# Optimization experiments

Measured on AMD Instinct MI355X. Metric: run time of the kernel, lower is better.

## Reference

```python
import jax, jax.numpy as jnp
import numpy as np

N_E = 8192
DIM = 256
BETA = 0.25


def _l2norm(x, eps=1e-12):
    # matches F.normalize(p=2, dim=-1): x / max(||x||, eps)
    n = jnp.sqrt(jnp.sum(x * x, axis=-1, keepdims=True))
    return x / jnp.maximum(n, eps)


def setup_inputs() -> dict:
    key = jax.random.key(0)
    k1, k2 = jax.random.split(key)
    z = jax.random.normal(k1, (8, 1024, DIM), dtype=jnp.float32)
    embedding_weight = jax.random.normal(k2, (N_E, DIM), dtype=jnp.float32)
    return {"z": z, "embedding_weight": embedding_weight}


def reference(z, embedding_weight):
    z = _l2norm(z)                                   # [B,S,D]
    zf = z.reshape(-1, DIM)                          # [N,D]
    embed_norm = _l2norm(embedding_weight)           # [n_e,D]
    # d = ||z||^2 + ||e||^2 - 2 z.e  -> [N, n_e]
    d = (jnp.sum(zf * zf, axis=1, keepdims=True)
         + jnp.sum(embed_norm * embed_norm, axis=1)
         - 2.0 * jnp.einsum('bd,nd->bn', zf, embed_norm))
    encoding_indices = jnp.argmin(d, axis=1).reshape(z.shape[:-1])  # [B,S]
    z_q = embedding_weight[encoding_indices]          # gather raw codes
    z_q = _l2norm(z_q)                                # [B,S,D]
    loss = (BETA * jnp.mean((jax.lax.stop_gradient(z_q) - z) ** 2)
            + jnp.mean((z_q - jax.lax.stop_gradient(z)) ** 2))
    z_q = z + jax.lax.stop_gradient(z_q - z)          # straight-through
    return z_q, loss, encoding_indices
```

## Files before the change

### kernel.cpp

```cpp
#include <hip/hip_runtime.h>
#include <hip/hip_fp16.h>
#include <cfloat>
#include <math.h>

#define DIM    256
#define N_TOK  8192
#define N_E    8192
#define NSEG   1024
#define MARGIN 0.012f

typedef __attribute__((ext_vector_type(8))) short bf16x8;
typedef __attribute__((ext_vector_type(4))) float f32x4;
typedef __attribute__((ext_vector_type(8))) unsigned short ushort8;

__device__ __forceinline__ unsigned short f2bf(float f) {
    unsigned u = __float_as_uint(f);
    unsigned r = u + 0x7fff + ((u >> 16) & 1);
    return (unsigned short)(r >> 16);
}
__device__ __forceinline__ unsigned fkey(float f) {
    unsigned u = __float_as_uint(f);
    return (u & 0x80000000u) ? ~u : (u | 0x80000000u);
}
__device__ __forceinline__ unsigned short f2h(float f) {
    const __half h = __float2half(f);
    return *(const unsigned short*)&h;
}
__device__ __forceinline__ float h2f(unsigned short u) {
    __half_raw r; r.x = u;
    return __half2float((__half)r);
}

__global__ __launch_bounds__(256) void l2norm_all(const float* __restrict__ z,
                                                  const float* __restrict__ emb,
                                                  float* __restrict__ zn,
                                                  unsigned short* __restrict__ zsw,
                                                  float* __restrict__ en,
                                                  unsigned short* __restrict__ esw,
                                                  float* __restrict__ e2) {
    const int lane = threadIdx.x & 63;
    const bool isE = blockIdx.x < (N_E / 4);
    const int row = (isE ? blockIdx.x : blockIdx.x - N_E / 4) * 4 + (threadIdx.x >> 6);
    const float* in = isE ? emb : z;
    float* out = isE ? en : zn;
    unsigned short* outb = isE ? esw : zsw;
    const float4 v = *(const float4*)(in + row * DIM + lane * 4);
    float s = v.x * v.x + v.y * v.y + v.z * v.z + v.w * v.w;
#pragma unroll
    for (int off = 1; off < 64; off <<= 1) s += __shfl_xor(s, off, 64);
    const float inv = 1.0f / fmaxf(sqrtf(s), 1e-12f);
    const float4 o = make_float4(v.x * inv, v.y * inv, v.z * inv, v.w * inv);
    *(float4*)(out + row * DIM + lane * 4) = o;
    ushort4 ob; ob.x = f2bf(o.x); ob.y = f2bf(o.y); ob.z = f2bf(o.z); ob.w = f2bf(o.w);
    {
        const int k0 = lane * 4;
        const size_t sidx = ((size_t)((row >> 4) * 8 + (k0 >> 5)) * 64
                             + ((k0 >> 3) & 3) * 16 + (row & 15)) * 8 + (k0 & 7);
        *(ushort4*)(outb + sidx) = ob;
    }
    if (isE) {
        float q = o.x * o.x + o.y * o.y + o.z * o.z + o.w * o.w;
#pragma unroll
        for (int off = 1; off < 64; off <<= 1) q += __shfl_xor(q, off, 64);
        if (lane == 0) e2[row] = q;
    }
}

__global__ __launch_bounds__(256, 3) void mfma_dist(const unsigned short* __restrict__ zsw,
                                                    const unsigned short* __restrict__ esw,
                                                    const float* __restrict__ e2,
                                                    unsigned short* __restrict__ segMh) {
    __shared__ float sm[16][128];

    const int tid  = threadIdx.x;
    const int lane = tid & 63;
    const int wave = tid >> 6;
    const int wm = wave & 1, wn = wave >> 1;
    const int row0 = (blockIdx.x & 63) * 128;
    const int col0 = (blockIdx.x >> 6) * 128;
    const int fr = lane & 15, q = lane >> 4;

    f32x4 acc[4][4];
#pragma unroll
    for (int ci = 0; ci < 4; ci++)
#pragma unroll
        for (int zi = 0; zi < 4; zi++) acc[ci][zi] = (f32x4){0.f, 0.f, 0.f, 0.f};

    const int aBase = (col0 >> 4) + wn * 4;
    const int bBase = (row0 >> 4) + wm * 4;
    auto la = [&](int i, int kc) {
        return *(const bf16x8*)(esw + (size_t)(aBase + i) * 4096 + kc * 512 + lane * 8);
    };
    auto lb = [&](int i, int kc) {
        return *(const bf16x8*)(zsw + (size_t)(bBase + i) * 4096 + kc * 512 + lane * 8);
    };

    bf16x8 ca[2][4], zb[2][4];
#pragma unroll
    for (int i = 0; i < 4; i++) { ca[0][i] = la(i, 0); zb[0][i] = lb(i, 0); }
#pragma unroll
    for (int kc = 0; kc < 8; kc++) {
        const int cur = kc & 1, nxt = cur ^ 1;
        if (kc < 7) {
#pragma unroll
            for (int i = 0; i < 4; i++) { ca[nxt][i] = la(i, kc + 1); zb[nxt][i] = lb(i, kc + 1); }
        }
#pragma unroll
        for (int ci = 0; ci < 4; ci++)
#pragma unroll
            for (int zi = 0; zi < 4; zi++)
                acc[ci][zi] = __builtin_amdgcn_mfma_f32_16x16x32_bf16(ca[cur][ci], zb[cur][zi], acc[ci][zi], 0, 0, 0);
    }

    float4 e2q[4];
#pragma unroll
    for (int ci = 0; ci < 4; ci++)
        e2q[ci] = *(const float4*)&e2[col0 + wn * 64 + ci * 16 + q * 4];
#pragma unroll
    for (int ci = 0; ci < 4; ci++) {
#pragma unroll
        for (int zi = 0; zi < 4; zi++) {
            const float t0 = fmaf(-2.0f, acc[ci][zi][0], e2q[ci].x);
            const float t1 = fmaf(-2.0f, acc[ci][zi][1], e2q[ci].y);
            const float t2 = fmaf(-2.0f, acc[ci][zi][2], e2q[ci].z);
            const float t3 = fmaf(-2.0f, acc[ci][zi][3], e2q[ci].w);
            float mm = fminf(fminf(t0, t1), fminf(t2, t3));
            mm = fminf(mm, __shfl_xor(mm, 16, 64));
            if (q == 0) sm[wn * 8 + ci * 2 + 0][wm * 64 + zi * 16 + fr] = mm;
            if (q == 2) sm[wn * 8 + ci * 2 + 1][wm * 64 + zi * 16 + fr] = mm;
        }
    }
    __syncthreads();
    {
        const int rl = tid & 127, part = tid >> 7;
        ushort8 o8;
#pragma unroll
        for (int j = 0; j < 8; j++) o8[j] = f2h(sm[part * 8 + j][rl]);
        *(ushort8*)&segMh[(size_t)(row0 + rl) * NSEG + (col0 >> 3) + part * 8] = o8;
    }
}

__global__ __launch_bounds__(256) void select_rescore(const unsigned short* __restrict__ segMh,
                                                      const float* __restrict__ en,
                                                      const float* __restrict__ e2,
                                                      float* zq,
                                                      float* out_base,
                                                      float* __restrict__ pl) {
    const int lane = threadIdx.x & 63;
    const int row  = (blockIdx.x << 2) + (threadIdx.x >> 6);
    const unsigned short* ph = segMh + (size_t)row * NSEG + lane * 16;
    const ushort8 u0 = *(const ushort8*)ph;
    const ushort8 u1 = *(const ushort8*)(ph + 8);
    float vv[16];
#pragma unroll
    for (int j = 0; j < 8; j++) { vv[j] = h2f(u0[j]); vv[8 + j] = h2f(u1[j]); }
    float m = vv[0];
#pragma unroll
    for (int j = 1; j < 16; j++) m = fminf(m, vv[j]);
#pragma unroll
    for (int off = 1; off < 64; off <<= 1) m = fminf(m, __shfl_xor(m, off, 64));
    const float thr = m + MARGIN;

    const int q = lane >> 4, f = lane & 15;
    const float4* zp = (const float4*)(zq + (size_t)row * DIM);
    float4 z4[4];
#pragma unroll
    for (int j = 0; j < 4; j++) z4[j] = zp[j * 16 + f];

    unsigned long long pk = ~0ull;
#pragma unroll
    for (int j = 0; j < 16; j++) {
        unsigned long long bal = __ballot(vv[j] <= thr);
        while (bal) {
            const int l = __ffsll(bal) - 1;
            bal &= bal - 1;
            const int seg = l * 16 + j;
#pragma unroll
            for (int g = 0; g < 2; g++) {
                const int col = seg * 8 + g * 4 + q;
                const float4* ep = (const float4*)(en + (size_t)col * DIM);
                float s = 0.f;
#pragma unroll
                for (int jj = 0; jj < 4; jj++) {
                    const float4 ev = ep[jj * 16 + f];
                    s = fmaf(z4[jj].x, ev.x, s); s = fmaf(z4[jj].y, ev.y, s);
                    s = fmaf(z4[jj].z, ev.z, s); s = fmaf(z4[jj].w, ev.w, s);
                }
#pragma unroll
                for (int off = 1; off < 16; off <<= 1) s += __shfl_xor(s, off, 64);
                const float d = fmaf(-2.0f, s, e2[col]);
                const unsigned long long key =
                    ((unsigned long long)fkey(d) << 32) | (unsigned)col;
                if (key < pk) pk = key;
            }
        }
    }
#pragma unroll
    for (int off = 16; off < 64; off <<= 1) {
        const unsigned long long o = __shfl_xor(pk, off, 64);
        if (o < pk) pk = o;
    }
    const int i = (int)(pk & 0xffffffffu);

    const float4 qv = *(const float4*)(en + (size_t)i * DIM + lane * 4);
    const float4 zv = *(const float4*)(zq + (size_t)row * DIM + lane * 4);
    const float dx = qv.x - zv.x, dy = qv.y - zv.y, dz = qv.z - zv.z, dw = qv.w - zv.w;
    float s = dx * dx + dy * dy + dz * dz + dw * dw;
    *(float4*)(zq + (size_t)row * DIM + lane * 4) = qv;
#pragma unroll
    for (int off = 1; off < 64; off <<= 1) s += __shfl_xor(s, off, 64);
    if (lane == 0) {
        pl[row] = s;
        out_base[N_TOK * DIM + 1 + row] = (float)i;
    }
}

__global__ __launch_bounds__(1024) void finalize_loss(const float* __restrict__ pl,
                                                      float* __restrict__ out) {
    __shared__ float sw[16];
    const int t = threadIdx.x;
    float s = 0.f;
#pragma unroll
    for (int j = 0; j < 8; j++) s += pl[t + j * 1024];
#pragma unroll
    for (int off = 1; off < 64; off <<= 1) s += __shfl_xor(s, off, 64);
    if ((t & 63) == 0) sw[t >> 6] = s;
    __syncthreads();
    if (t < 16) {
        float v = sw[t];
#pragma unroll
        for (int off = 1; off < 16; off <<= 1) v += __shfl_xor(v, off, 64);
        if (t == 0) out[N_TOK * DIM] = v * (1.25f / 2097152.0f);
    }
}

extern "C" void kernel_launch(void* const* d_in, const int* in_sizes, int n_in,
                              void* d_out, int out_size, void* d_ws, size_t ws_size,
                              hipStream_t stream) {
    const float* z   = (const float*)d_in[0];
    const float* emb = (const float*)d_in[1];
    float* out = (float*)d_out;
    char* ws = (char*)d_ws;

    float*          en    = (float*)(ws);
    unsigned short* esw   = (unsigned short*)(ws + 8388608);
    unsigned short* zsw   = (unsigned short*)(ws + 12582912);
    float*          e2    = (float*)(ws + 16777216);
    unsigned short* segMh = (unsigned short*)(ws + 16809984);
    float*          pl    = (float*)(ws + 33587200);

    l2norm_all<<<(N_E + N_TOK) / 4, 256, 0, stream>>>(z, emb, out, zsw, en, esw, e2);
    mfma_dist<<<64 * 64, 256, 0, stream>>>(zsw, esw, e2, segMh);
    select_rescore<<<N_TOK / 4, 256, 0, stream>>>(segMh, en, e2, out, out, pl);
    finalize_loss<<<1, 1024, 0, stream>>>(pl, out);
}
```

Measured before the change: 160.6 us.

## Stage token tile in LDS via global_load_lds instead of per-wave swizzled loads

The bf16 token matrix is now stored row-major rather than in the MFMA-swizzled layout. In the distance kernel, each block cooperatively loads its 128-row token tile slice for each k-chunk into shared memory with direct global-to-LDS loads, and waves read their B fragments from LDS. This is meant to cut redundant global/L2 reads of the token tile across the two waves that share it. In exchange it adds two block barriers per k-step, which serialise the loop and remove the previous register double-buffering for B.

```diff
diff --git a/kernel.cpp b/kernel.cpp
--- a/kernel.cpp
+++ b/kernel.cpp
@@ -34,7 +34,7 @@
 __global__ __launch_bounds__(256) void l2norm_all(const float* __restrict__ z,
                                                   const float* __restrict__ emb,
                                                   float* __restrict__ zn,
-                                                  unsigned short* __restrict__ zsw,
+                                                  unsigned short* __restrict__ zb,
                                                   float* __restrict__ en,
                                                   unsigned short* __restrict__ esw,
                                                   float* __restrict__ e2) {
@@ -43,7 +43,6 @@
     const int row = (isE ? blockIdx.x : blockIdx.x - N_E / 4) * 4 + (threadIdx.x >> 6);
     const float* in = isE ? emb : z;
     float* out = isE ? en : zn;
-    unsigned short* outb = isE ? esw : zsw;
     const float4 v = *(const float4*)(in + row * DIM + lane * 4);
     float s = v.x * v.x + v.y * v.y + v.z * v.z + v.w * v.w;
 #pragma unroll
@@ -52,24 +51,25 @@
     const float4 o = make_float4(v.x * inv, v.y * inv, v.z * inv, v.w * inv);
     *(float4*)(out + row * DIM + lane * 4) = o;
     ushort4 ob; ob.x = f2bf(o.x); ob.y = f2bf(o.y); ob.z = f2bf(o.z); ob.w = f2bf(o.w);
-    {
+    if (isE) {
         const int k0 = lane * 4;
         const size_t sidx = ((size_t)((row >> 4) * 8 + (k0 >> 5)) * 64
                              + ((k0 >> 3) & 3) * 16 + (row & 15)) * 8 + (k0 & 7);
-        *(ushort4*)(outb + sidx) = ob;
-    }
-    if (isE) {
+        *(ushort4*)(esw + sidx) = ob;
         float q = o.x * o.x + o.y * o.y + o.z * o.z + o.w * o.w;
 #pragma unroll
         for (int off = 1; off < 64; off <<= 1) q += __shfl_xor(q, off, 64);
         if (lane == 0) e2[row] = q;
-    }
-}
-
-__global__ __launch_bounds__(256, 3) void mfma_dist(const unsigned short* __restrict__ zsw,
+    } else {
+        *(ushort4*)(zb + row * DIM + lane * 4) = ob;
+    }
+}
+
+__global__ __launch_bounds__(256, 3) void mfma_dist(const unsigned short* __restrict__ zb,
                                                     const unsigned short* __restrict__ esw,
                                                     const float* __restrict__ e2,
                                                     unsigned short* __restrict__ segMh) {
+    __shared__ __align__(16) unsigned short As[128][32];
     __shared__ float sm[16][128];
 
     const int tid  = threadIdx.x;
@@ -87,29 +87,41 @@
         for (int zi = 0; zi < 4; zi++) acc[ci][zi] = (f32x4){0.f, 0.f, 0.f, 0.f};
 
     const int aBase = (col0 >> 4) + wn * 4;
-    const int bBase = (row0 >> 4) + wm * 4;
     auto la = [&](int i, int kc) {
         return *(const bf16x8*)(esw + (size_t)(aBase + i) * 4096 + kc * 512 + lane * 8);
     };
-    auto lb = [&](int i, int kc) {
-        return *(const bf16x8*)(zsw + (size_t)(bBase + i) * 4096 + kc * 512 + lane * 8);
-    };
-
-    bf16x8 ca[2][4], zb[2][4];
-#pragma unroll
-    for (int i = 0; i < 4; i++) { ca[0][i] = la(i, 0); zb[0][i] = lb(i, 0); }
+    const int srow  = lane >> 2;
+    const int skoff = (lane & 3) * 8;
+    const unsigned short* gZ = zb + (row0 + wave * 32 + srow) * DIM + skoff;
+
+    bf16x8 ca[2][4];
+#pragma unroll
+    for (int i = 0; i < 4; i++) ca[0][i] = la(i, 0);
+
 #pragma unroll
     for (int kc = 0; kc < 8; kc++) {
         const int cur = kc & 1, nxt = cur ^ 1;
         if (kc < 7) {
 #pragma unroll
-            for (int i = 0; i < 4; i++) { ca[nxt][i] = la(i, kc + 1); zb[nxt][i] = lb(i, kc + 1); }
-        }
+            for (int i = 0; i < 4; i++) ca[nxt][i] = la(i, kc + 1);
+        }
+        __syncthreads();
+#pragma unroll
+        for (int j = 0; j < 2; j++) {
+            __builtin_amdgcn_global_load_lds(
+                (const __attribute__((address_space(1))) unsigned int*)(gZ + j * 16 * DIM + kc * 32),
+                (__attribute__((address_space(3))) unsigned int*)&As[wave * 32 + j * 16][0],
+                16, 0, 0);
+        }
+        __syncthreads();
+        bf16x8 zfr[4];
+#pragma unroll
+        for (int i = 0; i < 4; i++) zfr[i] = *(const bf16x8*)&As[wm * 64 + i * 16 + fr][q * 8];
 #pragma unroll
         for (int ci = 0; ci < 4; ci++)
 #pragma unroll
             for (int zi = 0; zi < 4; zi++)
-                acc[ci][zi] = __builtin_amdgcn_mfma_f32_16x16x32_bf16(ca[cur][ci], zb[cur][zi], acc[ci][zi], 0, 0, 0);
+                acc[ci][zi] = __builtin_amdgcn_mfma_f32_16x16x32_bf16(ca[cur][ci], zfr[zi], acc[ci][zi], 0, 0, 0);
     }
 
     float4 e2q[4];
@@ -244,13 +256,13 @@
 
     float*          en    = (float*)(ws);
     unsigned short* esw   = (unsigned short*)(ws + 8388608);
-    unsigned short* zsw   = (unsigned short*)(ws + 12582912);
+    unsigned short* zb    = (unsigned short*)(ws + 12582912);
     float*          e2    = (float*)(ws + 16777216);
     unsigned short* segMh = (unsigned short*)(ws + 16809984);
     float*          pl    = (float*)(ws + 33587200);
 
-    l2norm_all<<<(N_E + N_TOK) / 4, 256, 0, stream>>>(z, emb, out, zsw, en, esw, e2);
-    mfma_dist<<<64 * 64, 256, 0, stream>>>(zsw, esw, e2, segMh);
+    l2norm_all<<<(N_E + N_TOK) / 4, 256, 0, stream>>>(z, emb, out, zb, en, esw, e2);
+    mfma_dist<<<64 * 64, 256, 0, stream>>>(zb, esw, e2, segMh);
     select_rescore<<<N_TOK / 4, 256, 0, stream>>>(segMh, en, e2, out, out, pl);
     finalize_loss<<<1, 1024, 0, stream>>>(pl, out);
 }
```

Result: faster. 138.9 us (-13.6%).
